# Performance work log

Hardware: AMD Instinct MI355X
Metric: run time of the kernel (lower is better)

The kernel has to match this reference:

```python
import jax, jax.numpy as jnp
from jax import lax
import numpy as np

BN_EPS = 1e-3  # keras BatchNormalization default epsilon


def setup_inputs() -> dict:
    key = jax.random.key(0)
    ks = jax.random.split(key, 7)
    B, T, Feat, Ch = 64, 4096, 32, 16
    kh, kw, F = 3, 32, 16
    return {
        "x": jax.random.normal(ks[0], (B, T, Feat, Ch), dtype=jnp.float32),
        "kernel": jax.random.normal(ks[1], (kh, kw, 1, F), dtype=jnp.float32) * 0.05,
        "bias": jax.random.normal(ks[2], (F,), dtype=jnp.float32) * 0.05,
        "gamma": jax.random.uniform(ks[3], (T,), dtype=jnp.float32),
        "beta": jax.random.normal(ks[4], (T,), dtype=jnp.float32) * 0.1,
        "moving_mean": jax.random.normal(ks[5], (T,), dtype=jnp.float32) * 0.1,
        "moving_var": jax.random.uniform(ks[6], (T,), dtype=jnp.float32),
    }


def reference(x, kernel, bias, gamma, beta, moving_mean, moving_var):
    # x: (B, T, Feat, Ch). Original loops over T, feeding (B, Ch, Feat, 1) to one
    # shared Conv2D; we batch all T timesteps into one conv call (same math).
    B, T, Feat, Ch = x.shape
    kh, kw, _, F = kernel.shape
    inp = jnp.transpose(x, (0, 1, 3, 2)).reshape(B * T, Ch, Feat, 1)  # (B*T, H=Ch, W=Feat, 1)
    y = lax.conv_general_dilated(
        inp, kernel, window_strides=(1, 1), padding="VALID",
        dimension_numbers=("NHWC", "HWIO", "NHWC"),
    ) + bias  # (B*T, Hp, Wp, F)
    Hp, Wp = y.shape[1], y.shape[2]  # Hp = Ch-kh+1, Wp = Feat-kw+1 (=1 here)
    # per-timestep transpose [0,1,3,2] -> (B, Hp, F, Wp), then concat over T on last axis
    y = y.reshape(B, T, Hp, Wp, F)
    y = jnp.transpose(y, (0, 2, 4, 1, 3)).reshape(B, Hp, F, T * Wp)
    # Dropout: identity at inference. BatchNormalization(axis=-1) in inference mode:
    y = (y - moving_mean) * (gamma / jnp.sqrt(moving_var + BN_EPS)) + beta
    y = jax.nn.relu(y)
    # not last layer: transpose [0,3,1,2] -> (B, T, Hp, F)
    return jnp.transpose(y, (0, 3, 1, 2))
```

## Files before the change

### kernel.cpp

```cpp
#include <hip/hip_runtime.h>
#include <hip/hip_bf16.h>


typedef __attribute__((ext_vector_type(8))) short bf16x8;
typedef __attribute__((ext_vector_type(4))) float f32x4;

#define NBT 16
#define XSTRIDE 40
#define XTILE (18 * XSTRIDE + 8)
#define WSTRIDE 104

__device__ __forceinline__ unsigned short f2bf(float f) {
    unsigned u = __builtin_bit_cast(unsigned, f);
    return (unsigned short)((u + 0x7fffu + ((u >> 16) & 1u)) >> 16);
}
__device__ __forceinline__ unsigned pack2(float a, float b) {
    return (unsigned)f2bf(a) | ((unsigned)f2bf(b) << 16);
}

__global__ __launch_bounds__(256) void tccnn_mfma(
    const float* __restrict__ x,
    const float* __restrict__ kern,
    const float* __restrict__ bias,
    const float* __restrict__ gamma,
    const float* __restrict__ beta,
    const float* __restrict__ mmean,
    const float* __restrict__ mvar,
    float* __restrict__ out)
{
    __shared__ __align__(16) unsigned short xs[NBT * XTILE];
    __shared__ __align__(16) unsigned short wsh[16 * WSTRIDE];

    const int tid = threadIdx.x;
    const long bt0 = (long)blockIdx.x * NBT;

    #pragma unroll
    for (int v = 0; v < 6; ++v) {
        int idx = v * 256 + tid;
        int ij = idx >> 4, f = idx & 15;
        wsh[f * WSTRIDE + ij] = f2bf(kern[idx]);
    }

    {
        int U = tid;
        int btl = U >> 4, u = U & 15;
        int cu = u & 3, ju = u >> 2;
        const float4* src = (const float4*)(x + (bt0 + btl) * 512 + ju * 128 + cu * 4);
        float4 r0 = src[0],  r1 = src[4],  r2 = src[8],  r3 = src[12];
        float4 r4 = src[16], r5 = src[20], r6 = src[24], r7 = src[28];
        unsigned short* dst = &xs[btl * XTILE + ju * 8];
        *(uint4*)&dst[(cu * 4 + 0) * XSTRIDE] = make_uint4(
            pack2(r0.x, r1.x), pack2(r2.x, r3.x), pack2(r4.x, r5.x), pack2(r6.x, r7.x));
        *(uint4*)&dst[(cu * 4 + 1) * XSTRIDE] = make_uint4(
            pack2(r0.y, r1.y), pack2(r2.y, r3.y), pack2(r4.y, r5.y), pack2(r6.y, r7.y));
        *(uint4*)&dst[(cu * 4 + 2) * XSTRIDE] = make_uint4(
            pack2(r0.z, r1.z), pack2(r2.z, r3.z), pack2(r4.z, r5.z), pack2(r6.z, r7.z));
        *(uint4*)&dst[(cu * 4 + 3) * XSTRIDE] = make_uint4(
            pack2(r0.w, r1.w), pack2(r2.w, r3.w), pack2(r4.w, r5.w), pack2(r6.w, r7.w));
    }
    __syncthreads();

    const int lane = tid & 63;
    const int wv = tid >> 6;
    const int hp = lane & 15;
    const int g = lane >> 4;

    bf16x8 bfr0 = *(const bf16x8*)&wsh[hp * WSTRIDE + 0 * 32 + g * 8];
    bf16x8 bfr1 = *(const bf16x8*)&wsh[hp * WSTRIDE + 1 * 32 + g * 8];
    bf16x8 bfr2 = *(const bf16x8*)&wsh[hp * WSTRIDE + 2 * 32 + g * 8];
    const float4 b4 = *(const float4*)&bias[g * 4];

    #pragma unroll
    for (int q = 0; q < 4; ++q) {
        const int btl = wv * 4 + q;
        const unsigned short* xt = &xs[btl * XTILE];
        bf16x8 a0 = *(const bf16x8*)&xt[(hp + 0) * XSTRIDE + g * 8];
        bf16x8 a1 = *(const bf16x8*)&xt[(hp + 1) * XSTRIDE + g * 8];
        bf16x8 a2 = *(const bf16x8*)&xt[(hp + 2) * XSTRIDE + g * 8];

        f32x4 acc = {0.f, 0.f, 0.f, 0.f};
        acc = __builtin_amdgcn_mfma_f32_16x16x32_bf16(bfr0, a0, acc, 0, 0, 0);
        acc = __builtin_amdgcn_mfma_f32_16x16x32_bf16(bfr1, a1, acc, 0, 0, 0);
        acc = __builtin_amdgcn_mfma_f32_16x16x32_bf16(bfr2, a2, acc, 0, 0, 0);

        const long bt = bt0 + btl;
        const int t = (int)(bt & 4095);
        const float sc = gamma[t] * rsqrtf(mvar[t] + 1e-3f);
        const float sh = beta[t] - mmean[t] * sc;

        if (hp < 14) {
            float4 y;
            y.x = fmaxf((acc[0] + b4.x) * sc + sh, 0.f);
            y.y = fmaxf((acc[1] + b4.y) * sc + sh, 0.f);
            y.z = fmaxf((acc[2] + b4.z) * sc + sh, 0.f);
            y.w = fmaxf((acc[3] + b4.w) * sc + sh, 0.f);
            *(float4*)(out + bt * 224 + hp * 16 + g * 4) = y;
        }
    }
}

extern "C" void kernel_launch(void* const* d_in, const int* in_sizes, int n_in,
                              void* d_out, int out_size, void* d_ws, size_t ws_size,
                              hipStream_t stream) {
    const float* x     = (const float*)d_in[0];
    const float* kern  = (const float*)d_in[1];
    const float* bias  = (const float*)d_in[2];
    const float* gamma = (const float*)d_in[3];
    const float* beta  = (const float*)d_in[4];
    const float* mmean = (const float*)d_in[5];
    const float* mvar  = (const float*)d_in[6];
    float* out = (float*)d_out;

    const int n_bt = 64 * 4096;
    const int blocks = n_bt / NBT;
    tccnn_mfma<<<blocks, 256, 0, stream>>>(x, kern, bias, gamma, beta,
                                           mmean, mvar, out);
}
```

Measured before the change: 140.8 us.

## Make blocks persistent over four tiles with register-prefetched next tile

New measurement: 154.2 us. 1.1x slower.

```diff
diff --git a/kernel.cpp b/kernel.cpp
--- a/kernel.cpp
+++ b/kernel.cpp
@@ -6,19 +6,20 @@
 typedef __attribute__((ext_vector_type(4))) float f32x4;
 
 #define NBT 16
+#define TPT 4
 #define XSTRIDE 40
 #define XTILE (18 * XSTRIDE + 8)
 #define WSTRIDE 104
 
 __device__ __forceinline__ unsigned short f2bf(float f) {
-    unsigned u = __builtin_bit_cast(unsigned, f);
-    return (unsigned short)((u + 0x7fffu + ((u >> 16) & 1u)) >> 16);
+    __hip_bfloat16 h = __float2bfloat16(f);
+    unsigned short s; __builtin_memcpy(&s, &h, 2); return s;
 }
 __device__ __forceinline__ unsigned pack2(float a, float b) {
     return (unsigned)f2bf(a) | ((unsigned)f2bf(b) << 16);
 }
 
-__global__ __launch_bounds__(256) void tccnn_mfma(
+__global__ __launch_bounds__(256, 4) void tccnn_mfma(
     const float* __restrict__ x,
     const float* __restrict__ kern,
     const float* __restrict__ bias,
@@ -30,9 +31,10 @@
 {
     __shared__ __align__(16) unsigned short xs[NBT * XTILE];
     __shared__ __align__(16) unsigned short wsh[16 * WSTRIDE];
+    __shared__ __align__(16) float scs[NBT], shs[NBT];
 
     const int tid = threadIdx.x;
-    const long bt0 = (long)blockIdx.x * NBT;
+    long btbase = (long)blockIdx.x * (NBT * TPT);
 
     #pragma unroll
     for (int v = 0; v < 6; ++v) {
@@ -41,61 +43,95 @@
         wsh[f * WSTRIDE + ij] = f2bf(kern[idx]);
     }
 
+    const int u = tid & 15, btl_s = tid >> 4;
+    const int cu = u & 3, ju = u >> 2;
+
+    float4 rr[8];
     {
-        int U = tid;
-        int btl = U >> 4, u = U & 15;
-        int cu = u & 3, ju = u >> 2;
-        const float4* src = (const float4*)(x + (bt0 + btl) * 512 + ju * 128 + cu * 4);
-        float4 r0 = src[0],  r1 = src[4],  r2 = src[8],  r3 = src[12];
-        float4 r4 = src[16], r5 = src[20], r6 = src[24], r7 = src[28];
-        unsigned short* dst = &xs[btl * XTILE + ju * 8];
-        *(uint4*)&dst[(cu * 4 + 0) * XSTRIDE] = make_uint4(
-            pack2(r0.x, r1.x), pack2(r2.x, r3.x), pack2(r4.x, r5.x), pack2(r6.x, r7.x));
-        *(uint4*)&dst[(cu * 4 + 1) * XSTRIDE] = make_uint4(
-            pack2(r0.y, r1.y), pack2(r2.y, r3.y), pack2(r4.y, r5.y), pack2(r6.y, r7.y));
-        *(uint4*)&dst[(cu * 4 + 2) * XSTRIDE] = make_uint4(
-            pack2(r0.z, r1.z), pack2(r2.z, r3.z), pack2(r4.z, r5.z), pack2(r6.z, r7.z));
-        *(uint4*)&dst[(cu * 4 + 3) * XSTRIDE] = make_uint4(
-            pack2(r0.w, r1.w), pack2(r2.w, r3.w), pack2(r4.w, r5.w), pack2(r6.w, r7.w));
+        const float4* src = (const float4*)(x + (btbase + btl_s) * 512 + ju * 128 + cu * 4);
+        #pragma unroll
+        for (int k = 0; k < 8; ++k) rr[k] = src[k * 4];
     }
+    float bn_g = 0.f, bn_b = 0.f, bn_m = 0.f, bn_v = 0.f;
+    if (tid < 16) {
+        int t = (int)((btbase + tid) & 4095);
+        bn_g = gamma[t]; bn_b = beta[t]; bn_m = mmean[t]; bn_v = mvar[t];
+    }
+
     __syncthreads();
 
-    const int lane = tid & 63;
-    const int wv = tid >> 6;
+    const int lane = tid & 63, wv = tid >> 6;
     const int hp = lane & 15;
     const int g = lane >> 4;
 
-    bf16x8 bfr0 = *(const bf16x8*)&wsh[hp * WSTRIDE + 0 * 32 + g * 8];
-    bf16x8 bfr1 = *(const bf16x8*)&wsh[hp * WSTRIDE + 1 * 32 + g * 8];
-    bf16x8 bfr2 = *(const bf16x8*)&wsh[hp * WSTRIDE + 2 * 32 + g * 8];
+    const bf16x8 bfr0 = *(const bf16x8*)&wsh[hp * WSTRIDE + 0 * 32 + g * 8];
+    const bf16x8 bfr1 = *(const bf16x8*)&wsh[hp * WSTRIDE + 1 * 32 + g * 8];
+    const bf16x8 bfr2 = *(const bf16x8*)&wsh[hp * WSTRIDE + 2 * 32 + g * 8];
     const float4 b4 = *(const float4*)&bias[g * 4];
 
-    #pragma unroll
-    for (int q = 0; q < 4; ++q) {
-        const int btl = wv * 4 + q;
-        const unsigned short* xt = &xs[btl * XTILE];
-        bf16x8 a0 = *(const bf16x8*)&xt[(hp + 0) * XSTRIDE + g * 8];
-        bf16x8 a1 = *(const bf16x8*)&xt[(hp + 1) * XSTRIDE + g * 8];
-        bf16x8 a2 = *(const bf16x8*)&xt[(hp + 2) * XSTRIDE + g * 8];
+    for (int tt = 0; tt < TPT; ++tt) {
+        if (tid < 16) {
+            float sc = bn_g * rsqrtf(bn_v + 1e-3f);
+            scs[tid] = sc;
+            shs[tid] = bn_b - bn_m * sc;
+        }
+        {
+            unsigned short* dst = &xs[btl_s * XTILE + ju * 8];
+            *(uint4*)&dst[(cu * 4 + 0) * XSTRIDE] = make_uint4(
+                pack2(rr[0].x, rr[1].x), pack2(rr[2].x, rr[3].x),
+                pack2(rr[4].x, rr[5].x), pack2(rr[6].x, rr[7].x));
+            *(uint4*)&dst[(cu * 4 + 1) * XSTRIDE] = make_uint4(
+                pack2(rr[0].y, rr[1].y), pack2(rr[2].y, rr[3].y),
+                pack2(rr[4].y, rr[5].y), pack2(rr[6].y, rr[7].y));
+            *(uint4*)&dst[(cu * 4 + 2) * XSTRIDE] = make_uint4(
+                pack2(rr[0].z, rr[1].z), pack2(rr[2].z, rr[3].z),
+                pack2(rr[4].z, rr[5].z), pack2(rr[6].z, rr[7].z));
+            *(uint4*)&dst[(cu * 4 + 3) * XSTRIDE] = make_uint4(
+                pack2(rr[0].w, rr[1].w), pack2(rr[2].w, rr[3].w),
+                pack2(rr[4].w, rr[5].w), pack2(rr[6].w, rr[7].w));
+        }
+        __syncthreads();
 
-        f32x4 acc = {0.f, 0.f, 0.f, 0.f};
-        acc = __builtin_amdgcn_mfma_f32_16x16x32_bf16(bfr0, a0, acc, 0, 0, 0);
-        acc = __builtin_amdgcn_mfma_f32_16x16x32_bf16(bfr1, a1, acc, 0, 0, 0);
-        acc = __builtin_amdgcn_mfma_f32_16x16x32_bf16(bfr2, a2, acc, 0, 0, 0);
+        if (tt + 1 < TPT) {
+            const float4* src = (const float4*)(x + (btbase + NBT + btl_s) * 512 + ju * 128 + cu * 4);
+            #pragma unroll
+            for (int k = 0; k < 8; ++k) rr[k] = src[k * 4];
+            if (tid < 16) {
+                int t = (int)((btbase + NBT + tid) & 4095);
+                bn_g = gamma[t]; bn_b = beta[t]; bn_m = mmean[t]; bn_v = mvar[t];
+            }
+        }
 
-        const long bt = bt0 + btl;
-        const int t = (int)(bt & 4095);
-        const float sc = gamma[t] * rsqrtf(mvar[t] + 1e-3f);
-        const float sh = beta[t] - mmean[t] * sc;
+        const float4 sc4 = *(const float4*)&scs[wv * 4];
+        const float4 sh4 = *(const float4*)&shs[wv * 4];
+        const float scq[4] = {sc4.x, sc4.y, sc4.z, sc4.w};
+        const float shq[4] = {sh4.x, sh4.y, sh4.z, sh4.w};
 
-        if (hp < 14) {
-            float4 y;
-            y.x = fmaxf((acc[0] + b4.x) * sc + sh, 0.f);
-            y.y = fmaxf((acc[1] + b4.y) * sc + sh, 0.f);
-            y.z = fmaxf((acc[2] + b4.z) * sc + sh, 0.f);
-            y.w = fmaxf((acc[3] + b4.w) * sc + sh, 0.f);
-            *(float4*)(out + bt * 224 + hp * 16 + g * 4) = y;
+        #pragma unroll
+        for (int q = 0; q < 4; ++q) {
+            const int btl = wv * 4 + q;
+            const unsigned short* xt = &xs[btl * XTILE];
+            bf16x8 a0 = *(const bf16x8*)&xt[(hp + 0) * XSTRIDE + g * 8];
+            bf16x8 a1 = *(const bf16x8*)&xt[(hp + 1) * XSTRIDE + g * 8];
+            bf16x8 a2 = *(const bf16x8*)&xt[(hp + 2) * XSTRIDE + g * 8];
+
+            f32x4 acc = {0.f, 0.f, 0.f, 0.f};
+            acc = __builtin_amdgcn_mfma_f32_16x16x32_bf16(bfr0, a0, acc, 0, 0, 0);
+            acc = __builtin_amdgcn_mfma_f32_16x16x32_bf16(bfr1, a1, acc, 0, 0, 0);
+            acc = __builtin_amdgcn_mfma_f32_16x16x32_bf16(bfr2, a2, acc, 0, 0, 0);
+
+            const float sc = scq[q], sh = shq[q];
+            if (hp < 14) {
+                float4 y;
+                y.x = fmaxf((acc[0] + b4.x) * sc + sh, 0.f);
+                y.y = fmaxf((acc[1] + b4.y) * sc + sh, 0.f);
+                y.z = fmaxf((acc[2] + b4.z) * sc + sh, 0.f);
+                y.w = fmaxf((acc[3] + b4.w) * sc + sh, 0.f);
+                *(float4*)(out + (btbase + btl) * 224 + hp * 16 + g * 4) = y;
+            }
         }
+        __syncthreads();
+        btbase += NBT;
     }
 }
 
@@ -112,7 +148,7 @@
     float* out = (float*)d_out;
 
     const int n_bt = 64 * 4096;
-    const int blocks = n_bt / NBT;
+    const int blocks = n_bt / (NBT * TPT);
     tccnn_mfma<<<blocks, 256, 0, stream>>>(x, kern, bias, gamma, beta,
                                            mmean, mvar, out);
 }
```

## Load weights directly to registers, shrink LDS tile, use nontemporal loads/stores

Applied to the files above, without the earlier changes.

New measurement: 147.7 us. +4.9%, slower.

```diff
diff --git a/kernel.cpp b/kernel.cpp
--- a/kernel.cpp
+++ b/kernel.cpp
@@ -4,11 +4,11 @@
 
 typedef __attribute__((ext_vector_type(8))) short bf16x8;
 typedef __attribute__((ext_vector_type(4))) float f32x4;
+typedef __attribute__((ext_vector_type(4))) unsigned int u32x4;
 
 #define NBT 16
 #define XSTRIDE 40
-#define XTILE (18 * XSTRIDE + 8)
-#define WSTRIDE 104
+#define XTILE (16 * XSTRIDE)
 
 __device__ __forceinline__ unsigned short f2bf(float f) {
     unsigned u = __builtin_bit_cast(unsigned, f);
@@ -18,7 +18,7 @@
     return (unsigned)f2bf(a) | ((unsigned)f2bf(b) << 16);
 }
 
-__global__ __launch_bounds__(256) void tccnn_mfma(
+__global__ __launch_bounds__(256, 8) void tccnn_mfma(
     const float* __restrict__ x,
     const float* __restrict__ kern,
     const float* __restrict__ bias,
@@ -29,59 +29,69 @@
     float* __restrict__ out)
 {
     __shared__ __align__(16) unsigned short xs[NBT * XTILE];
-    __shared__ __align__(16) unsigned short wsh[16 * WSTRIDE];
 
     const int tid = threadIdx.x;
     const long bt0 = (long)blockIdx.x * NBT;
 
-    #pragma unroll
-    for (int v = 0; v < 6; ++v) {
-        int idx = v * 256 + tid;
-        int ij = idx >> 4, f = idx & 15;
-        wsh[f * WSTRIDE + ij] = f2bf(kern[idx]);
+    {
+        const int u = tid & 15, btl_s = tid >> 4;
+        const int cu = u & 3, ju = u >> 2;
+        const float* xbase = x + (bt0 + btl_s) * 512 + cu * 4;
+        unsigned short* dst = &xs[btl_s * XTILE + ju * 8];
+        #pragma unroll
+        for (int p = 0; p < 2; ++p) {
+            const int j0 = ju * 8 + p * 4;
+            const f32x4* s4 = (const f32x4*)(xbase + j0 * 16);
+            f32x4 r0 = __builtin_nontemporal_load(s4 + 0);
+            f32x4 r1 = __builtin_nontemporal_load(s4 + 4);
+            f32x4 r2 = __builtin_nontemporal_load(s4 + 8);
+            f32x4 r3 = __builtin_nontemporal_load(s4 + 12);
+            *(uint2*)&dst[(cu * 4 + 0) * XSTRIDE + p * 4] =
+                make_uint2(pack2(r0.x, r1.x), pack2(r2.x, r3.x));
+            *(uint2*)&dst[(cu * 4 + 1) * XSTRIDE + p * 4] =
+                make_uint2(pack2(r0.y, r1.y), pack2(r2.y, r3.y));
+            *(uint2*)&dst[(cu * 4 + 2) * XSTRIDE + p * 4] =
+                make_uint2(pack2(r0.z, r1.z), pack2(r2.z, r3.z));
+            *(uint2*)&dst[(cu * 4 + 3) * XSTRIDE + p * 4] =
+                make_uint2(pack2(r0.w, r1.w), pack2(r2.w, r3.w));
+        }
     }
-
-    {
-        int U = tid;
-        int btl = U >> 4, u = U & 15;
-        int cu = u & 3, ju = u >> 2;
-        const float4* src = (const float4*)(x + (bt0 + btl) * 512 + ju * 128 + cu * 4);
-        float4 r0 = src[0],  r1 = src[4],  r2 = src[8],  r3 = src[12];
-        float4 r4 = src[16], r5 = src[20], r6 = src[24], r7 = src[28];
-        unsigned short* dst = &xs[btl * XTILE + ju * 8];
-        *(uint4*)&dst[(cu * 4 + 0) * XSTRIDE] = make_uint4(
-            pack2(r0.x, r1.x), pack2(r2.x, r3.x), pack2(r4.x, r5.x), pack2(r6.x, r7.x));
-        *(uint4*)&dst[(cu * 4 + 1) * XSTRIDE] = make_uint4(
-            pack2(r0.y, r1.y), pack2(r2.y, r3.y), pack2(r4.y, r5.y), pack2(r6.y, r7.y));
-        *(uint4*)&dst[(cu * 4 + 2) * XSTRIDE] = make_uint4(
-            pack2(r0.z, r1.z), pack2(r2.z, r3.z), pack2(r4.z, r5.z), pack2(r6.z, r7.z));
-        *(uint4*)&dst[(cu * 4 + 3) * XSTRIDE] = make_uint4(
-            pack2(r0.w, r1.w), pack2(r2.w, r3.w), pack2(r4.w, r5.w), pack2(r6.w, r7.w));
-    }
-    __syncthreads();
 
     const int lane = tid & 63;
     const int wv = tid >> 6;
     const int hp = lane & 15;
     const int g = lane >> 4;
 
-    bf16x8 bfr0 = *(const bf16x8*)&wsh[hp * WSTRIDE + 0 * 32 + g * 8];
-    bf16x8 bfr1 = *(const bf16x8*)&wsh[hp * WSTRIDE + 1 * 32 + g * 8];
-    bf16x8 bfr2 = *(const bf16x8*)&wsh[hp * WSTRIDE + 2 * 32 + g * 8];
+    bf16x8 bfr[3];
+    #pragma unroll
+    for (int i = 0; i < 3; ++i) {
+        const float* kb = kern + (i * 32 + g * 8) * 16 + hp;
+        u32x4 w;
+        #pragma unroll
+        for (int jj = 0; jj < 4; ++jj)
+            w[jj] = pack2(kb[(2 * jj) * 16], kb[(2 * jj + 1) * 16]);
+        bfr[i] = __builtin_bit_cast(bf16x8, w);
+    }
     const float4 b4 = *(const float4*)&bias[g * 4];
+
+    __syncthreads();
+
+    const int row0 = hp * XSTRIDE + g * 8;
+    const int row1 = (hp < 15 ? hp + 1 : 15) * XSTRIDE + g * 8;
+    const int row2 = (hp < 14 ? hp + 2 : 15) * XSTRIDE + g * 8;
 
     #pragma unroll
     for (int q = 0; q < 4; ++q) {
         const int btl = wv * 4 + q;
         const unsigned short* xt = &xs[btl * XTILE];
-        bf16x8 a0 = *(const bf16x8*)&xt[(hp + 0) * XSTRIDE + g * 8];
-        bf16x8 a1 = *(const bf16x8*)&xt[(hp + 1) * XSTRIDE + g * 8];
-        bf16x8 a2 = *(const bf16x8*)&xt[(hp + 2) * XSTRIDE + g * 8];
+        bf16x8 a0 = *(const bf16x8*)&xt[row0];
+        bf16x8 a1 = *(const bf16x8*)&xt[row1];
+        bf16x8 a2 = *(const bf16x8*)&xt[row2];
 
         f32x4 acc = {0.f, 0.f, 0.f, 0.f};
-        acc = __builtin_amdgcn_mfma_f32_16x16x32_bf16(bfr0, a0, acc, 0, 0, 0);
-        acc = __builtin_amdgcn_mfma_f32_16x16x32_bf16(bfr1, a1, acc, 0, 0, 0);
-        acc = __builtin_amdgcn_mfma_f32_16x16x32_bf16(bfr2, a2, acc, 0, 0, 0);
+        acc = __builtin_amdgcn_mfma_f32_16x16x32_bf16(bfr[0], a0, acc, 0, 0, 0);
+        acc = __builtin_amdgcn_mfma_f32_16x16x32_bf16(bfr[1], a1, acc, 0, 0, 0);
+        acc = __builtin_amdgcn_mfma_f32_16x16x32_bf16(bfr[2], a2, acc, 0, 0, 0);
 
         const long bt = bt0 + btl;
         const int t = (int)(bt & 4095);
@@ -89,12 +99,12 @@
         const float sh = beta[t] - mmean[t] * sc;
 
         if (hp < 14) {
-            float4 y;
+            f32x4 y;
             y.x = fmaxf((acc[0] + b4.x) * sc + sh, 0.f);
             y.y = fmaxf((acc[1] + b4.y) * sc + sh, 0.f);
             y.z = fmaxf((acc[2] + b4.z) * sc + sh, 0.f);
             y.w = fmaxf((acc[3] + b4.w) * sc + sh, 0.f);
-            *(float4*)(out + bt * 224 + hp * 16 + g * 4) = y;
+            __builtin_nontemporal_store(y, (f32x4*)(out + bt * 224 + hp * 16 + g * 4));
         }
     }
 }
```
